# Kernel optimization log

Hardware: AMD Instinct MI355X
Metric: run time of the kernel (lower is better)

Reference implementation:

```python
import jax, jax.numpy as jnp
import numpy as np

HIDDEN = 2048
NUM_HEADS = 16
HEAD_DIM = HIDDEN // NUM_HEADS
BATCH, SEQ = 2, 2048


def setup_inputs() -> dict:
    key = jax.random.key(0)
    ks = jax.random.split(key, 9)
    s = 1.0 / np.sqrt(HIDDEN)
    return {
        "hidden_state": jax.random.normal(ks[0], (BATCH, SEQ, HIDDEN), dtype=jnp.float32),
        "Wq": jax.random.normal(ks[1], (HIDDEN, HIDDEN), dtype=jnp.float32) * s,
        "bq": jax.random.normal(ks[2], (HIDDEN,), dtype=jnp.float32) * 0.01,
        "Wk": jax.random.normal(ks[3], (HIDDEN, HIDDEN), dtype=jnp.float32) * s,
        "bk": jax.random.normal(ks[4], (HIDDEN,), dtype=jnp.float32) * 0.01,
        "Wv": jax.random.normal(ks[5], (HIDDEN, HIDDEN), dtype=jnp.float32) * s,
        "bv": jax.random.normal(ks[6], (HIDDEN,), dtype=jnp.float32) * 0.01,
        "Wo": jax.random.normal(ks[7], (HIDDEN, HIDDEN), dtype=jnp.float32) * s,
        "bo": jax.random.normal(ks[8], (HIDDEN,), dtype=jnp.float32) * 0.01,
    }


def _split_heads(x):
    # (B, S, H*D) -> (B, H, S, D)
    b, s, _ = x.shape
    return x.reshape(b, s, NUM_HEADS, HEAD_DIM).transpose(0, 2, 1, 3)


def reference(hidden_state, Wq, bq, Wk, bk, Wv, bv, Wo, bo):
    q = _split_heads(hidden_state @ Wq + bq)
    k = _split_heads(hidden_state @ Wk + bk)
    v = _split_heads(hidden_state @ Wv + bv)
    scale = 1.0 / jnp.sqrt(jnp.asarray(HEAD_DIM, dtype=hidden_state.dtype))
    scores = jnp.einsum("bhqd,bhkd->bhqk", q, k) * scale  # (B,H,S,S)
    probs = jax.nn.softmax(scores, axis=-1)
    out = jnp.einsum("bhqk,bhkd->bhqd", probs, v)  # (B,H,S,D)
    b, h, s, d = out.shape
    out = out.transpose(0, 2, 1, 3).reshape(b, s, h * d)  # merge heads
    return out @ Wo + bo
```

## Files before the change

### kernel.cpp

```cpp
#include <hip/hip_runtime.h>
#include <math.h>

typedef __bf16 bf16;
typedef __bf16 bf16x4 __attribute__((ext_vector_type(4)));
typedef __bf16 bf16x8 __attribute__((ext_vector_type(8)));
typedef float  f32x4  __attribute__((ext_vector_type(4)));

#define HIDDEN 2048
#define NH     16
#define HD     128
#define BATCH  2
#define SEQ    2048
#define MROWS  (BATCH*SEQ)
#define NQKV   (3*HIDDEN)

__device__ __forceinline__ void async16(const bf16* g, bf16* l) {
  __builtin_amdgcn_global_load_lds(
      (const __attribute__((address_space(1))) void*)g,
      (__attribute__((address_space(3))) void*)l, 16, 0, 0);
}

__global__ __launch_bounds__(256) void prep_kernel(
    const float* __restrict__ hs,
    const float* __restrict__ Wq, const float* __restrict__ Wk,
    const float* __restrict__ Wv, const float* __restrict__ Wo,
    const float* __restrict__ bq, const float* __restrict__ bk,
    const float* __restrict__ bv,
    bf16* __restrict__ Abf, bf16* __restrict__ WtQKV, bf16* __restrict__ WtO,
    float* __restrict__ biasQ) {
  const int z = blockIdx.z;
  if (z < 4) {
    const float* src; bf16* dst;
    switch (z) {
      case 0: src = Wq; dst = WtQKV; break;
      case 1: src = Wk; dst = WtQKV + 2048 * 2048; break;
      case 2: src = Wv; dst = WtQKV + 2 * 2048 * 2048; break;
      default: src = Wo; dst = WtO; break;
    }
    __shared__ float t[32][33];
    int x  = blockIdx.x * 32 + threadIdx.x;
    int y0 = blockIdx.y * 32;
#pragma unroll
    for (int i = 0; i < 32; i += 8)
      t[threadIdx.y + i][threadIdx.x] = src[(size_t)(y0 + threadIdx.y + i) * HIDDEN + x];
    __syncthreads();
    int xo  = blockIdx.y * 32 + threadIdx.x;
    int yo0 = blockIdx.x * 32;
#pragma unroll
    for (int i = 0; i < 32; i += 8)
      dst[(size_t)(yo0 + threadIdx.y + i) * HIDDEN + xo] = (bf16)t[threadIdx.x][threadIdx.y + i];
  } else {
    const int bid = blockIdx.y * 64 + blockIdx.x;
    const int tid = threadIdx.y * 32 + threadIdx.x;
    int base = bid * 512 + tid;
#pragma unroll
    for (int p = 0; p < 2; p++) {
      float4 f = ((const float4*)hs)[base + p * 256];
      bf16x4 o;
      o[0] = (bf16)f.x; o[1] = (bf16)f.y; o[2] = (bf16)f.z; o[3] = (bf16)f.w;
      ((bf16x4*)Abf)[base + p * 256] = o;
    }
    if (bid < 24) {
      int i = bid * 256 + tid;
      biasQ[i] = (i < 2048) ? bq[i] : (i < 4096 ? bk[i - 2048] : bv[i - 4096]);
    }
  }
}

__global__ __launch_bounds__(256) void transpose_v_kernel(
    const bf16* __restrict__ QKV, bf16* __restrict__ Vt) {
  __shared__ bf16 t[32][33];
  int bh = blockIdx.z, b = bh >> 4, h = bh & 15;
  const bf16* src = QKV + (size_t)b * SEQ * NQKV + 2 * HIDDEN + h * HD;
  bf16* dst = Vt + (size_t)bh * HD * SEQ;
  int s0 = blockIdx.x * 32, d0 = blockIdx.y * 32;
#pragma unroll
  for (int i = 0; i < 32; i += 8)
    t[threadIdx.y + i][threadIdx.x] = src[(size_t)(s0 + threadIdx.y + i) * NQKV + d0 + threadIdx.x];
  __syncthreads();
#pragma unroll
  for (int i = 0; i < 32; i += 8)
    dst[(size_t)(d0 + threadIdx.y + i) * SEQ + s0 + threadIdx.x] = t[threadIdx.x][threadIdx.y + i];
}

template <typename OutT>
__global__ __launch_bounds__(256) void gemm_bt_bias(
    const bf16* __restrict__ A, const bf16* __restrict__ Bt,
    const float* __restrict__ bias, OutT* __restrict__ C, int N, int K) {
  __shared__ bf16 Ash[128 * 64];
  __shared__ bf16 Bsh[128 * 64];
  const int tid = threadIdx.x;
  const int wave = tid >> 6, lane = tid & 63, quad = lane >> 4, l16 = lane & 15;
  const int wm = (wave & 1) * 64, wn = (wave >> 1) * 64;
  const int m0 = blockIdx.x * 128, n0 = blockIdx.y * 128;

  const f32x4 zero4 = {0.f, 0.f, 0.f, 0.f};
  f32x4 acc[4][4];
#pragma unroll
  for (int i = 0; i < 4; i++)
#pragma unroll
    for (int j = 0; j < 4; j++) acc[i][j] = zero4;

  const int crow = tid >> 3, ccc = tid & 7;
  const int cd = (ccc - crow) & 7;
  const int l7 = l16 & 7;

  const bf16* pa[4];
  const bf16* pb[4];
#pragma unroll
  for (int s = 0; s < 4; s++) {
    pa[s] = &A[(size_t)(m0 + s * 32 + crow) * K + cd * 8];
    pb[s] = &Bt[(size_t)(n0 + s * 32 + crow) * K + cd * 8];
  }

  for (int kt = 0; kt < K; kt += 64) {
    __syncthreads();
#pragma unroll
    for (int s = 0; s < 4; s++) {
      async16(pa[s], &Ash[s * 2048 + tid * 8]);
      async16(pb[s], &Bsh[s * 2048 + tid * 8]);
      pa[s] += 64; pb[s] += 64;
    }
    __syncthreads();

#pragma unroll
    for (int kk = 0; kk < 2; kk++) {
      const int pc = (kk * 4 + quad + l7) & 7;
      bf16x8 af[4], bfr[4];
#pragma unroll
      for (int i = 0; i < 4; i++) af[i]  = *(const bf16x8*)&Ash[(wm + i * 16 + l16) * 64 + pc * 8];
#pragma unroll
      for (int j = 0; j < 4; j++) bfr[j] = *(const bf16x8*)&Bsh[(wn + j * 16 + l16) * 64 + pc * 8];
#pragma unroll
      for (int i = 0; i < 4; i++)
#pragma unroll
        for (int j = 0; j < 4; j++)
          acc[i][j] = __builtin_amdgcn_mfma_f32_16x16x32_bf16(af[i], bfr[j], acc[i][j], 0, 0, 0);
    }
  }

#pragma unroll
  for (int i = 0; i < 4; i++)
#pragma unroll
    for (int j = 0; j < 4; j++) {
      int n = n0 + wn + j * 16 + l16;
      float bv = bias[n];
#pragma unroll
      for (int r = 0; r < 4; r++) {
        int m = m0 + wm + i * 16 + quad * 4 + r;
        C[(size_t)m * N + n] = (OutT)(acc[i][j][r] + bv);
      }
    }
}

#define KTS   64

__global__ __launch_bounds__(256, 2) void flash_attn_kernel(
    const bf16* __restrict__ QKV, const bf16* __restrict__ Vt, bf16* __restrict__ O) {
  const int fid = blockIdx.x + 16 * blockIdx.y;
  const int nid = (fid & 7) * 64 + (fid >> 3);
  const int bh = nid >> 4, b = bh >> 4, h = bh & 15;
  const int q0 = (nid & 15) * 128;
  const int tid = threadIdx.x, wave = tid >> 6, lane = tid & 63, quad = lane >> 4, l16 = lane & 15;

  const bf16* Qb  = QKV + (size_t)b * SEQ * NQKV + h * HD;
  const bf16* Kb  = QKV + (size_t)b * SEQ * NQKV + HIDDEN + h * HD;
  const bf16* Vtb = Vt + (size_t)bh * HD * SEQ;

  __shared__ bf16 Ksh[2][KTS * HD];
  __shared__ bf16 Vsh[2][HD * KTS];
  __shared__ bf16 Psh[128 * 64];

  const int qrow = q0 + wave * 32;
  const float sc = 0.08838834764831845f * 1.44269504088896340f;

  bf16x8 qf[2][4];
#pragma unroll
  for (int mt = 0; mt < 2; mt++)
#pragma unroll
    for (int kk = 0; kk < 4; kk++) {
      bf16x8 t = *(const bf16x8*)&Qb[(size_t)(qrow + mt * 16 + l16) * NQKV + kk * 32 + quad * 8];
#pragma unroll
      for (int j = 0; j < 8; j++) t[j] = (bf16)((float)t[j] * sc);
      qf[mt][kk] = t;
    }

  const f32x4 zero4 = {0.f, 0.f, 0.f, 0.f};
  f32x4 oacc[2][8];
#pragma unroll
  for (int mt = 0; mt < 2; mt++)
#pragma unroll
    for (int nt = 0; nt < 8; nt++) oacc[mt][nt] = zero4;

  float lrun[2] = {0.f, 0.f};

  const int krp = tid >> 4, kpp = tid & 15;
  const int vrp = tid >> 3, vpp = tid & 7;
  const int l7 = l16 & 7;

  const bf16* pk[4];
  const bf16* pv[4];
#pragma unroll
  for (int s = 0; s < 4; s++) {
    int r  = s * 16 + krp;
    pk[s] = &Kb[(size_t)r * NQKV + (kpp ^ (r & 7)) * 8];
    int rv = s * 32 + vrp;
    pv[s] = &Vtb[(size_t)rv * SEQ + (vpp ^ (rv & 7)) * 8];
  }

#pragma unroll
  for (int s = 0; s < 4; s++) {
    async16(pk[s], &Ksh[0][s * 2048 + tid * 8]);
    async16(pv[s], &Vsh[0][s * 2048 + tid * 8]);
    pk[s] += (size_t)KTS * NQKV;
    pv[s] += KTS;
  }

  const int NT = SEQ / KTS;
  for (int t = 0; t < NT; ++t) {
    const int cur = t & 1;
    if (t + 1 < NT) {
#pragma unroll
      for (int s = 0; s < 4; s++) {
        async16(pk[s], &Ksh[cur ^ 1][s * 2048 + tid * 8]);
        async16(pv[s], &Vsh[cur ^ 1][s * 2048 + tid * 8]);
        pk[s] += (size_t)KTS * NQKV;
        pv[s] += KTS;
      }
      asm volatile("s_waitcnt vmcnt(8)" ::: "memory");
    } else {
      asm volatile("s_waitcnt vmcnt(0)" ::: "memory");
    }
    __builtin_amdgcn_s_barrier();

    f32x4 st[2][4];
#pragma unroll
    for (int mt = 0; mt < 2; mt++)
#pragma unroll
      for (int nt = 0; nt < 4; nt++) st[mt][nt] = zero4;
#pragma unroll
    for (int kk = 0; kk < 4; kk++) {
      const int p = (4 * kk + quad) ^ l7;
      bf16x8 kf[4];
#pragma unroll
      for (int nt = 0; nt < 4; nt++)
        kf[nt] = *(const bf16x8*)&Ksh[cur][(nt * 16 + l16) * HD + p * 8];
      __builtin_amdgcn_s_setprio(1);
#pragma unroll
      for (int mt = 0; mt < 2; mt++)
#pragma unroll
        for (int nt = 0; nt < 4; nt++)
          st[mt][nt] = __builtin_amdgcn_mfma_f32_16x16x32_bf16(kf[nt], qf[mt][kk], st[mt][nt], 0, 0, 0);
      __builtin_amdgcn_s_setprio(0);
    }

    float rs[2] = {0.f, 0.f};
#pragma unroll
    for (int mt = 0; mt < 2; mt++)
#pragma unroll
      for (int nt = 0; nt < 4; nt++) {
        bf16x4 pk4;
#pragma unroll
        for (int r = 0; r < 4; r++) {
          float p = exp2f(st[mt][nt][r]);
          rs[mt] += p;
          pk4[r] = (bf16)p;
        }
        int pbyte = ((wave * 32 + mt * 16 + l16) * 64 + nt * 16 + quad * 4) * 2;
        pbyte ^= (l16 & 7) << 4;
        *(bf16x4*)((char*)Psh + pbyte) = pk4;
      }
#pragma unroll
    for (int mt = 0; mt < 2; mt++) {
      float t2 = rs[mt];
      t2 += __shfl_xor(t2, 16);
      t2 += __shfl_xor(t2, 32);
      lrun[mt] += t2;
    }

#pragma unroll
    for (int kk2 = 0; kk2 < 2; kk2++) {
      bf16x8 pf[2], vf[8];
#pragma unroll
      for (int mt = 0; mt < 2; mt++) {
        int pbyte = ((wave * 32 + mt * 16 + l16) * 64 + kk2 * 32 + quad * 8) * 2;
        pbyte ^= (l16 & 7) << 4;
        pf[mt] = *(const bf16x8*)((char*)Psh + pbyte);
      }
#pragma unroll
      for (int nt = 0; nt < 8; nt++) {
        int p = (4 * kk2 + quad) ^ l7;
        vf[nt] = *(const bf16x8*)&Vsh[cur][(nt * 16 + l16) * KTS + p * 8];
      }
      __builtin_amdgcn_s_setprio(1);
#pragma unroll
      for (int mt = 0; mt < 2; mt++)
#pragma unroll
        for (int nt = 0; nt < 8; nt++)
          oacc[mt][nt] = __builtin_amdgcn_mfma_f32_16x16x32_bf16(pf[mt], vf[nt], oacc[mt][nt], 0, 0, 0);
      __builtin_amdgcn_s_setprio(0);
    }

    __builtin_amdgcn_s_barrier();
  }

#pragma unroll
  for (int mt = 0; mt < 2; mt++) {
    float inv[4];
#pragma unroll
    for (int r = 0; r < 4; r++)
      inv[r] = 1.0f / __shfl(lrun[mt], (lane & 48) | (quad * 4 + r));
#pragma unroll
    for (int nt = 0; nt < 8; nt++)
#pragma unroll
      for (int r = 0; r < 4; r++) {
        int q = qrow + mt * 16 + quad * 4 + r;
        int d = nt * 16 + l16;
        O[(size_t)(b * SEQ + q) * HIDDEN + h * HD + d] = (bf16)(oacc[mt][nt][r] * inv[r]);
      }
  }
}

extern "C" void kernel_launch(void* const* d_in, const int* in_sizes, int n_in,
                              void* d_out, int out_size, void* d_ws, size_t ws_size,
                              hipStream_t stream) {
  const float* hs = (const float*)d_in[0];
  const float* Wq = (const float*)d_in[1];
  const float* bq = (const float*)d_in[2];
  const float* Wk = (const float*)d_in[3];
  const float* bk = (const float*)d_in[4];
  const float* Wv = (const float*)d_in[5];
  const float* bv = (const float*)d_in[6];
  const float* Wo = (const float*)d_in[7];
  const float* bo = (const float*)d_in[8];
  float* out = (float*)d_out;

  char* ws = (char*)d_ws;
  bf16*  Abf   = (bf16*)(ws);
  bf16*  WtQKV = (bf16*)(ws + 16777216);
  bf16*  WtO   = (bf16*)(ws + 41943040);
  float* biasQ = (float*)(ws + 50331648);
  bf16*  QKV   = (bf16*)(ws + 50356224);
  bf16*  VT    = (bf16*)(ws + 100687872);
  bf16*  Obf   = (bf16*)(ws + 117465088);

  dim3 tb(32, 8);
  prep_kernel<<<dim3(64, 64, 5), tb, 0, stream>>>(
      hs, Wq, Wk, Wv, Wo, bq, bk, bv,
      Abf, WtQKV, WtO, biasQ);

  gemm_bt_bias<bf16><<<dim3(32, 48), 256, 0, stream>>>(Abf, WtQKV, biasQ, QKV, NQKV, HIDDEN);
  transpose_v_kernel<<<dim3(64, 4, 32), tb, 0, stream>>>(QKV, VT);
  flash_attn_kernel<<<dim3(16, 32), 256, 0, stream>>>(QKV, VT, Obf);
  gemm_bt_bias<float><<<dim3(32, 16), 256, 0, stream>>>(Obf, WtO, bo, out, HIDDEN, HIDDEN);
}
```

Baseline: 403.0 us.

## Use two-wave flash attention blocks with 64 query rows per wave, single-buffered K/V

The attention kernel shrinks from four waves of 32 query rows to two waves of 64 rows each, so each loaded K/V fragment feeds twice as many MFMAs. The K/V double buffer is removed in favour of one LDS buffer, loaded synchronously with __syncthreads before and after each tile. The goal is more register-level reuse and less LDS per block, at the price of much higher register pressure, lower occupancy, and no overlap of global loads with compute.

Result: slower. 432.7 us (+7.4%).

```diff
diff --git a/kernel.cpp b/kernel.cpp
--- a/kernel.cpp
+++ b/kernel.cpp
@@ -155,7 +155,7 @@
 
 #define KTS   64
 
-__global__ __launch_bounds__(256, 2) void flash_attn_kernel(
+__global__ __launch_bounds__(128, 1) void flash_attn_kernel(
     const bf16* __restrict__ QKV, const bf16* __restrict__ Vt, bf16* __restrict__ O) {
   const int fid = blockIdx.x + 16 * blockIdx.y;
   const int nid = (fid & 7) * 64 + (fid >> 3);
@@ -167,16 +167,17 @@
   const bf16* Kb  = QKV + (size_t)b * SEQ * NQKV + HIDDEN + h * HD;
   const bf16* Vtb = Vt + (size_t)bh * HD * SEQ;
 
-  __shared__ bf16 Ksh[2][KTS * HD];
-  __shared__ bf16 Vsh[2][HD * KTS];
+  __shared__ bf16 Ksh[KTS * HD];
+  __shared__ bf16 Vsh[HD * KTS];
   __shared__ bf16 Psh[128 * 64];
 
-  const int qrow = q0 + wave * 32;
+  const int qrow = q0 + wave * 64;
   const float sc = 0.08838834764831845f * 1.44269504088896340f;
-
-  bf16x8 qf[2][4];
-#pragma unroll
-  for (int mt = 0; mt < 2; mt++)
+  const int l7 = l16 & 7;
+
+  bf16x8 qf[4][4];
+#pragma unroll
+  for (int mt = 0; mt < 4; mt++)
 #pragma unroll
     for (int kk = 0; kk < 4; kk++) {
       bf16x8 t = *(const bf16x8*)&Qb[(size_t)(qrow + mt * 16 + l16) * NQKV + kk * 32 + quad * 8];
@@ -186,56 +187,34 @@
     }
 
   const f32x4 zero4 = {0.f, 0.f, 0.f, 0.f};
-  f32x4 oacc[2][8];
-#pragma unroll
-  for (int mt = 0; mt < 2; mt++)
+  f32x4 oacc[4][8];
+#pragma unroll
+  for (int mt = 0; mt < 4; mt++)
 #pragma unroll
     for (int nt = 0; nt < 8; nt++) oacc[mt][nt] = zero4;
 
-  float lrun[2] = {0.f, 0.f};
+  float lrun[4] = {0.f, 0.f, 0.f, 0.f};
 
   const int krp = tid >> 4, kpp = tid & 15;
   const int vrp = tid >> 3, vpp = tid & 7;
-  const int l7 = l16 & 7;
-
-  const bf16* pk[4];
-  const bf16* pv[4];
-#pragma unroll
-  for (int s = 0; s < 4; s++) {
-    int r  = s * 16 + krp;
-    pk[s] = &Kb[(size_t)r * NQKV + (kpp ^ (r & 7)) * 8];
-    int rv = s * 32 + vrp;
-    pv[s] = &Vtb[(size_t)rv * SEQ + (vpp ^ (rv & 7)) * 8];
-  }
-
-#pragma unroll
-  for (int s = 0; s < 4; s++) {
-    async16(pk[s], &Ksh[0][s * 2048 + tid * 8]);
-    async16(pv[s], &Vsh[0][s * 2048 + tid * 8]);
-    pk[s] += (size_t)KTS * NQKV;
-    pv[s] += KTS;
-  }
-
-  const int NT = SEQ / KTS;
-  for (int t = 0; t < NT; ++t) {
-    const int cur = t & 1;
-    if (t + 1 < NT) {
-#pragma unroll
-      for (int s = 0; s < 4; s++) {
-        async16(pk[s], &Ksh[cur ^ 1][s * 2048 + tid * 8]);
-        async16(pv[s], &Vsh[cur ^ 1][s * 2048 + tid * 8]);
-        pk[s] += (size_t)KTS * NQKV;
-        pv[s] += KTS;
-      }
-      asm volatile("s_waitcnt vmcnt(8)" ::: "memory");
-    } else {
-      asm volatile("s_waitcnt vmcnt(0)" ::: "memory");
-    }
-    __builtin_amdgcn_s_barrier();
-
-    f32x4 st[2][4];
-#pragma unroll
-    for (int mt = 0; mt < 2; mt++)
+
+  const bf16* pk0 = Kb  + (size_t)krp * NQKV + (kpp ^ (krp & 7)) * 8;
+  const bf16* pv0 = Vtb + (size_t)vrp * SEQ  + (vpp ^ (vrp & 7)) * 8;
+
+  for (int kt = 0; kt < SEQ; kt += KTS) {
+    __syncthreads();
+#pragma unroll
+    for (int s = 0; s < 8; s++) {
+      async16(pk0 + (size_t)s * 8 * NQKV, &Ksh[s * 1024 + tid * 8]);
+      async16(pv0 + (size_t)s * 16 * SEQ, &Vsh[s * 1024 + tid * 8]);
+    }
+    pk0 += (size_t)KTS * NQKV;
+    pv0 += KTS;
+    __syncthreads();
+
+    f32x4 st[4][4];
+#pragma unroll
+    for (int mt = 0; mt < 4; mt++)
 #pragma unroll
       for (int nt = 0; nt < 4; nt++) st[mt][nt] = zero4;
 #pragma unroll
@@ -244,68 +223,61 @@
       bf16x8 kf[4];
 #pragma unroll
       for (int nt = 0; nt < 4; nt++)
-        kf[nt] = *(const bf16x8*)&Ksh[cur][(nt * 16 + l16) * HD + p * 8];
+        kf[nt] = *(const bf16x8*)&Ksh[(nt * 16 + l16) * HD + p * 8];
       __builtin_amdgcn_s_setprio(1);
 #pragma unroll
-      for (int mt = 0; mt < 2; mt++)
+      for (int mt = 0; mt < 4; mt++)
 #pragma unroll
         for (int nt = 0; nt < 4; nt++)
           st[mt][nt] = __builtin_amdgcn_mfma_f32_16x16x32_bf16(kf[nt], qf[mt][kk], st[mt][nt], 0, 0, 0);
       __builtin_amdgcn_s_setprio(0);
     }
 
-    float rs[2] = {0.f, 0.f};
-#pragma unroll
-    for (int mt = 0; mt < 2; mt++)
+#pragma unroll
+    for (int mt = 0; mt < 4; mt++) {
+      float rs = 0.f;
 #pragma unroll
       for (int nt = 0; nt < 4; nt++) {
         bf16x4 pk4;
 #pragma unroll
         for (int r = 0; r < 4; r++) {
           float p = exp2f(st[mt][nt][r]);
-          rs[mt] += p;
+          rs += p;
           pk4[r] = (bf16)p;
         }
-        int pbyte = ((wave * 32 + mt * 16 + l16) * 64 + nt * 16 + quad * 4) * 2;
+        int pbyte = ((wave * 64 + mt * 16 + l16) * 64 + nt * 16 + quad * 4) * 2;
         pbyte ^= (l16 & 7) << 4;
         *(bf16x4*)((char*)Psh + pbyte) = pk4;
       }
-#pragma unroll
-    for (int mt = 0; mt < 2; mt++) {
-      float t2 = rs[mt];
-      t2 += __shfl_xor(t2, 16);
-      t2 += __shfl_xor(t2, 32);
-      lrun[mt] += t2;
+      rs += __shfl_xor(rs, 16);
+      rs += __shfl_xor(rs, 32);
+      lrun[mt] += rs;
     }
 
 #pragma unroll
     for (int kk2 = 0; kk2 < 2; kk2++) {
-      bf16x8 pf[2], vf[8];
-#pragma unroll
-      for (int mt = 0; mt < 2; mt++) {
-        int pbyte = ((wave * 32 + mt * 16 + l16) * 64 + kk2 * 32 + quad * 8) * 2;
-        pbyte ^= (l16 & 7) << 4;
-        pf[mt] = *(const bf16x8*)((char*)Psh + pbyte);
-      }
+      bf16x8 vf[8];
 #pragma unroll
       for (int nt = 0; nt < 8; nt++) {
         int p = (4 * kk2 + quad) ^ l7;
-        vf[nt] = *(const bf16x8*)&Vsh[cur][(nt * 16 + l16) * KTS + p * 8];
-      }
-      __builtin_amdgcn_s_setprio(1);
-#pragma unroll
-      for (int mt = 0; mt < 2; mt++)
+        vf[nt] = *(const bf16x8*)&Vsh[(nt * 16 + l16) * KTS + p * 8];
+      }
+#pragma unroll
+      for (int mt = 0; mt < 4; mt++) {
+        int pbyte = ((wave * 64 + mt * 16 + l16) * 64 + kk2 * 32 + quad * 8) * 2;
+        pbyte ^= (l16 & 7) << 4;
+        bf16x8 pf = *(const bf16x8*)((char*)Psh + pbyte);
+        __builtin_amdgcn_s_setprio(1);
 #pragma unroll
         for (int nt = 0; nt < 8; nt++)
-          oacc[mt][nt] = __builtin_amdgcn_mfma_f32_16x16x32_bf16(pf[mt], vf[nt], oacc[mt][nt], 0, 0, 0);
-      __builtin_amdgcn_s_setprio(0);
-    }
-
-    __builtin_amdgcn_s_barrier();
-  }
-
-#pragma unroll
-  for (int mt = 0; mt < 2; mt++) {
+          oacc[mt][nt] = __builtin_amdgcn_mfma_f32_16x16x32_bf16(pf, vf[nt], oacc[mt][nt], 0, 0, 0);
+        __builtin_amdgcn_s_setprio(0);
+      }
+    }
+  }
+
+#pragma unroll
+  for (int mt = 0; mt < 4; mt++) {
     float inv[4];
 #pragma unroll
     for (int r = 0; r < 4; r++)
@@ -351,6 +323,6 @@
 
   gemm_bt_bias<bf16><<<dim3(32, 48), 256, 0, stream>>>(Abf, WtQKV, biasQ, QKV, NQKV, HIDDEN);
   transpose_v_kernel<<<dim3(64, 4, 32), tb, 0, stream>>>(QKV, VT);
-  flash_attn_kernel<<<dim3(16, 32), 256, 0, stream>>>(QKV, VT, Obf);
+  flash_attn_kernel<<<dim3(16, 32), 128, 0, stream>>>(QKV, VT, Obf);
   gemm_bt_bias<float><<<dim3(32, 16), 256, 0, stream>>>(Obf, WtO, bo, out, HIDDEN, HIDDEN);
 }
```
